# Kernel optimization log

Hardware: AMD Instinct MI355X
Metric: run time of the kernel (lower is better)

The kernel has to match this reference:

```python
import jax, jax.numpy as jnp
import numpy as np

N_NODES = 100000
N_EDGES = 1600000
IN_FEAT = 256
HIDDEN = 64
N_CLASSES = 16


def gcn_conv(x, edge_index, W, b):
    """PyG GCNConv: add self-loops, symmetric normalization, linear+aggregate."""
    n = x.shape[0]
    src, dst = edge_index[0], edge_index[1]
    loops = jnp.arange(n, dtype=src.dtype)
    src = jnp.concatenate([src, loops])
    dst = jnp.concatenate([dst, loops])
    # in-degree on graph with self-loops
    deg = jax.ops.segment_sum(jnp.ones(src.shape[0], dtype=x.dtype), dst, num_segments=n)
    dinv = jnp.where(deg > 0, jax.lax.rsqrt(deg), 0.0)
    h = x @ W                                  # [N, out]
    norm = dinv[src] * dinv[dst]               # [E+N]
    msg = h[src] * norm[:, None]                # gather + scale (memory-bound)
    out = jax.ops.segment_sum(msg, dst, num_segments=n)  # scatter-add
    return out + b


def setup_inputs() -> dict:
    key = jax.random.key(0)
    ks = jax.random.split(key, 5)
    x = jax.random.normal(ks[0], (N_NODES, IN_FEAT), dtype=jnp.float32)
    edge_index = jax.random.randint(ks[1], (2, N_EDGES), 0, N_NODES, dtype=jnp.int64)
    W1 = jax.random.normal(ks[2], (IN_FEAT, HIDDEN), dtype=jnp.float32) * (1.0 / np.sqrt(IN_FEAT))
    b1 = jnp.zeros((HIDDEN,), dtype=jnp.float32)
    W2 = jax.random.normal(ks[3], (HIDDEN, N_CLASSES), dtype=jnp.float32) * (1.0 / np.sqrt(HIDDEN))
    b2 = jnp.zeros((N_CLASSES,), dtype=jnp.float32)
    return {"x": x, "edge_index": edge_index, "W1": W1, "b1": b1, "W2": W2, "b2": b2}


def reference(x, edge_index, W1, b1, W2, b2):
    h = gcn_conv(x, edge_index, W1, b1)
    h = jax.nn.relu(h)
    # dropout p=0.5 is identity in eval mode (training=False)
    out = gcn_conv(h, edge_index, W2, b2)
    return out
```

## Files before the change

kernel.cpp:

```cpp
#include <hip/hip_runtime.h>

#define NN 100000
#define NE 1600000
#define FIN 256
#define FH 64
#define FC 16

#define SCAN_CHUNK 1024
#define NB_SCAN ((NN + SCAN_CHUNK - 1) / SCAN_CHUNK)
#define NB_COUNT ((NE / 4 + 255) / 256)
#define NB_GEMM1 ((NN + 127) / 128)
#define NB_FUSED (3 * NB_GEMM1)

typedef int v2i __attribute__((ext_vector_type(2)));
typedef int v4i __attribute__((ext_vector_type(4)));
typedef short s16x8 __attribute__((ext_vector_type(8)));
typedef float f32x4 __attribute__((ext_vector_type(4)));

__device__ __forceinline__ float4 fma4(float4 v, float w, float4 a) {
    a.x = fmaf(v.x, w, a.x); a.y = fmaf(v.y, w, a.y);
    a.z = fmaf(v.z, w, a.z); a.w = fmaf(v.w, w, a.w);
    return a;
}
__device__ __forceinline__ float4 add4(float4 a, float4 v) {
    a.x += v.x; a.y += v.y; a.z += v.z; a.w += v.w;
    return a;
}
__device__ __forceinline__ float4 xor_add4(float4 r, int m) {
    r.x += __shfl_xor(r.x, m, 64); r.y += __shfl_xor(r.y, m, 64);
    r.z += __shfl_xor(r.z, m, 64); r.w += __shfl_xor(r.w, m, 64);
    return r;
}

__device__ __forceinline__ unsigned short bf16rne(float f) {
    unsigned u = __float_as_uint(f);
    u += 0x7FFFu + ((u >> 16) & 1u);
    return (unsigned short)(u >> 16);
}

__device__ __forceinline__ void split8(const float* f, s16x8& hi, s16x8& lo) {
    #pragma unroll
    for (int i = 0; i < 8; i++) {
        unsigned u = __float_as_uint(f[i]);
        unsigned short h = (unsigned short)((u + 0x7FFFu + ((u >> 16) & 1u)) >> 16);
        float l = f[i] - __uint_as_float((unsigned)h << 16);
        unsigned ul = __float_as_uint(l);
        hi[i] = (short)h;
        lo[i] = (short)((ul + 0x7FFFu + ((ul >> 16) & 1u)) >> 16);
    }
}

__global__ __launch_bounds__(256) void prep_k(const int* __restrict__ ei,
                                              int* __restrict__ flag,
                                              const float* __restrict__ W,
                                              unsigned short* __restrict__ Whi,
                                              unsigned short* __restrict__ Wlo) {
    int b = blockIdx.x;
    if (b == 8) {
        if (threadIdx.x == 0) {
            int z = (ei[1] == 0) & (ei[3] == 0) & (ei[5] == 0) & (ei[7] == 0);
            *flag = z;
        }
        return;
    }
    int slot = b * 256 + threadIdx.x;
    int l = slot & 63;
    int c = (slot >> 6) & 3;
    int s = slot >> 8;
    int k0 = s * 32 + (l >> 4) * 8;
    int col = c * 16 + (l & 15);
    #pragma unroll
    for (int i = 0; i < 8; i++) {
        float f = W[(k0 + i) * FH + col];
        unsigned short h = bf16rne(f);
        float lres = f - __uint_as_float((unsigned)h << 16);
        Whi[slot * 8 + i] = h;
        Wlo[slot * 8 + i] = bf16rne(lres);
    }
}

__global__ __launch_bounds__(256, 4) void fused_k(const int* __restrict__ ei,
                                                  const int* __restrict__ flag,
                                                  int* __restrict__ deg,
                                                  v2i* __restrict__ packed,
                                                  const float* __restrict__ x,
                                                  const unsigned short* __restrict__ Whi,
                                                  const unsigned short* __restrict__ Wlo,
                                                  float* __restrict__ h1) {
    const int b = blockIdx.x;
    if ((b % 3) != 2) {
        int cb = (b / 3) * 2 + (b % 3);
        if (cb >= NB_COUNT) return;
        int e = (cb * 256 + threadIdx.x) * 4;
        if (e >= NE) return;
        int f = *flag;
        int s0, s1, s2, s3, d0, d1, d2, d3;
        if (f) {
            v4i a = *(const v4i*)&ei[2 * e];
            v4i b2 = *(const v4i*)&ei[2 * e + 4];
            s0 = a.x; s1 = a.z; s2 = b2.x; s3 = b2.z;
            v4i c = *(const v4i*)&ei[2 * (NE + e)];
            v4i d = *(const v4i*)&ei[2 * (NE + e) + 4];
            d0 = c.x; d1 = c.z; d2 = d.x; d3 = d.z;
        } else {
            v4i a = *(const v4i*)&ei[e];
            s0 = a.x; s1 = a.y; s2 = a.z; s3 = a.w;
            v4i c = *(const v4i*)&ei[NE + e];
            d0 = c.x; d1 = c.y; d2 = c.z; d3 = c.w;
        }
        int r0 = atomicAdd(&deg[d0], 1);
        int r1 = atomicAdd(&deg[d1], 1);
        int r2 = atomicAdd(&deg[d2], 1);
        int r3 = atomicAdd(&deg[d3], 1);
        v4i pa, pb;
        pa.x = s0; pa.y = d0 | (r0 << 17);
        pa.z = s1; pa.w = d1 | (r1 << 17);
        pb.x = s2; pb.y = d2 | (r2 << 17);
        pb.z = s3; pb.w = d3 | (r3 << 17);
        *(v4i*)&packed[e] = pa;
        *(v4i*)&packed[e + 2] = pb;
        return;
    }
    const int t = threadIdx.x;
    const int lane = t & 63;
    const int wid = t >> 6;
    const int mb = (b / 3) * 128 + wid * 32;
    const int lr = lane & 15;
    const int lk = (lane >> 4) * 8;

    int ra0 = mb + lr;
    int ra1 = mb + 16 + lr;
    const float* pa0 = x + (size_t)(ra0 < NN ? ra0 : NN - 1) * FIN + lk;
    const float* pa1 = x + (size_t)(ra1 < NN ? ra1 : NN - 1) * FIN + lk;

    f32x4 acc[2][4] = {};

    for (int s = 0; s < 8; s++) {
        float fa0[8], fa1[8];
        float4 q;
        q = *(const float4*)(pa0 + s * 32);
        fa0[0] = q.x; fa0[1] = q.y; fa0[2] = q.z; fa0[3] = q.w;
        q = *(const float4*)(pa0 + s * 32 + 4);
        fa0[4] = q.x; fa0[5] = q.y; fa0[6] = q.z; fa0[7] = q.w;
        q = *(const float4*)(pa1 + s * 32);
        fa1[0] = q.x; fa1[1] = q.y; fa1[2] = q.z; fa1[3] = q.w;
        q = *(const float4*)(pa1 + s * 32 + 4);
        fa1[4] = q.x; fa1[5] = q.y; fa1[6] = q.z; fa1[7] = q.w;

        s16x8 a0h, a0l, a1h, a1l;
        split8(fa0, a0h, a0l);
        split8(fa1, a1h, a1l);

        #pragma unroll
        for (int c = 0; c < 4; c++) {
            s16x8 wh = *(const s16x8*)&Whi[((s * 4 + c) * 64 + lane) * 8];
            s16x8 wl = *(const s16x8*)&Wlo[((s * 4 + c) * 64 + lane) * 8];
            acc[0][c] = __builtin_amdgcn_mfma_f32_16x16x32_bf16(a0h, wh, acc[0][c], 0, 0, 0);
            acc[0][c] = __builtin_amdgcn_mfma_f32_16x16x32_bf16(a0l, wh, acc[0][c], 0, 0, 0);
            acc[0][c] = __builtin_amdgcn_mfma_f32_16x16x32_bf16(a0h, wl, acc[0][c], 0, 0, 0);
            acc[1][c] = __builtin_amdgcn_mfma_f32_16x16x32_bf16(a1h, wh, acc[1][c], 0, 0, 0);
            acc[1][c] = __builtin_amdgcn_mfma_f32_16x16x32_bf16(a1l, wh, acc[1][c], 0, 0, 0);
            acc[1][c] = __builtin_amdgcn_mfma_f32_16x16x32_bf16(a1h, wl, acc[1][c], 0, 0, 0);
        }
    }
    #pragma unroll
    for (int r = 0; r < 2; r++) {
        int rowb = mb + 16 * r + (lane >> 4) * 4;
        #pragma unroll
        for (int c = 0; c < 4; c++) {
            #pragma unroll
            for (int v = 0; v < 4; v++) {
                int row = rowb + v;
                if (row < NN)
                    h1[(size_t)row * FH + 16 * c + lr] = acc[r][c][v];
            }
        }
    }
}

__global__ __launch_bounds__(256) void scan_sum_k(const int* __restrict__ deg,
                                                  int* __restrict__ partial,
                                                  float* __restrict__ dinv,
                                                  float* __restrict__ h1) {
    __shared__ int red[256];
    __shared__ float sdv[SCAN_CHUNK];
    int b = blockIdx.x, t = threadIdx.x;
    int base = b * SCAN_CHUNK + t * 4;
    int s = 0;
    #pragma unroll
    for (int i = 0; i < 4; i++) {
        int idx = base + i;
        float dv = 0.f;
        if (idx < NN) {
            int d = deg[idx];
            s += d;
            dv = rsqrtf((float)(d + 1));
            dinv[idx] = dv;
        }
        sdv[t * 4 + i] = dv;
    }
    red[t] = s;
    __syncthreads();
    #pragma unroll 4
    for (int it = 0; it < 64; it++) {
        int q = it * 256 + t;
        int rl = q >> 4;
        int row = b * SCAN_CHUNK + rl;
        if (row < NN) {
            float d = sdv[rl];
            float4 v = *(const float4*)&h1[(size_t)row * FH + (q & 15) * 4];
            v.x *= d; v.y *= d; v.z *= d; v.w *= d;
            *(float4*)&h1[(size_t)row * FH + (q & 15) * 4] = v;
        }
    }
    for (int off = 128; off > 0; off >>= 1) {
        if (t < off) red[t] += red[t + off];
        __syncthreads();
    }
    if (t == 0) partial[b] = red[0];
}

__global__ __launch_bounds__(128) void scan_part_k(int* __restrict__ partial) {
    __shared__ int s[128];
    int t = threadIdx.x;
    int v = (t < NB_SCAN) ? partial[t] : 0;
    s[t] = v; __syncthreads();
    for (int off = 1; off < 128; off <<= 1) {
        int u = (t >= off) ? s[t - off] : 0;
        __syncthreads();
        s[t] += u;
        __syncthreads();
    }
    if (t < NB_SCAN) partial[t] = s[t] - v;
}

__global__ __launch_bounds__(256) void scan_out_k(const int* __restrict__ deg,
                                                  const int* __restrict__ partial,
                                                  int* __restrict__ row_start) {
    __shared__ int s[256];
    int b = blockIdx.x, t = threadIdx.x;
    int base = b * SCAN_CHUNK + t * 4;
    int v[4]; int sum = 0;
    #pragma unroll
    for (int i = 0; i < 4; i++) {
        int idx = base + i;
        v[i] = (idx < NN) ? deg[idx] : 0;
        sum += v[i];
    }
    s[t] = sum; __syncthreads();
    for (int off = 1; off < 256; off <<= 1) {
        int u = (t >= off) ? s[t - off] : 0;
        __syncthreads();
        s[t] += u;
        __syncthreads();
    }
    int run = partial[b] + s[t] - sum;
    #pragma unroll
    for (int i = 0; i < 4; i++) {
        int idx = base + i;
        if (idx < NN) {
            row_start[idx] = run;
            run += v[i];
            if (idx == NN - 1) row_start[NN] = run;
        }
    }
}

__global__ __launch_bounds__(256) void fill_k(const int* __restrict__ packed,
                                              const int* __restrict__ row_start,
                                              int* __restrict__ csr) {
    int e = (blockIdx.x * 256 + threadIdx.x) * 2;
    if (e >= NE) return;
    v4i p = __builtin_nontemporal_load((const v4i*)&packed[2 * e]);
    int d0 = p.y & 0x1FFFF;
    int r0 = ((unsigned)p.y) >> 17;
    int d1 = p.w & 0x1FFFF;
    int r1 = ((unsigned)p.w) >> 17;
    csr[row_start[d0] + r0] = p.x;
    csr[row_start[d1] + r1] = p.z;
}

__global__ __launch_bounds__(256) void agg1g_k(const int* __restrict__ csr,
                                               const int* __restrict__ row_start,
                                               const float* __restrict__ h1,
                                               const float* __restrict__ dinv,
                                               const float* __restrict__ b1,
                                               const float* __restrict__ W2,
                                               float* __restrict__ h2) {
    __shared__ float sW2[FH * FC];
    __shared__ float sp[4][FH];
    const int t = threadIdx.x;
    #pragma unroll
    for (int i = 0; i < 4; i++) sW2[t + 256 * i] = W2[t + 256 * i];
    __syncthreads();

    int wid = t >> 6;
    int n = blockIdx.x * 4 + wid;
    int lane = t & 63;
    if (n >= NN) return;
    int sg = lane >> 4;
    int fl = lane & 15;
    int s0 = row_start[n], s1 = row_start[n + 1];
    float4 A = make_float4(0.f, 0.f, 0.f, 0.f);
    float4 B = make_float4(0.f, 0.f, 0.f, 0.f);
    float4 C = make_float4(0.f, 0.f, 0.f, 0.f);
    float4 D = make_float4(0.f, 0.f, 0.f, 0.f);
    for (int j0 = s0; j0 < s1; j0 += 64) {
        int idx = j0 + lane;
        int sl = (idx < s1) ? csr[idx] : 0;
        int cnt = s1 - j0; if (cnt > 64) cnt = 64;
        int j = 0;
        for (; j + 16 <= cnt; j += 16) {
            int eA = __shfl(sl, j + sg, 64);
            int eB = __shfl(sl, j + 4 + sg, 64);
            int eC = __shfl(sl, j + 8 + sg, 64);
            int eD = __shfl(sl, j + 12 + sg, 64);
            float4 vA = *(const float4*)&h1[eA * FH + fl * 4];
            float4 vB = *(const float4*)&h1[eB * FH + fl * 4];
            float4 vC = *(const float4*)&h1[eC * FH + fl * 4];
            float4 vD = *(const float4*)&h1[eD * FH + fl * 4];
            A = add4(A, vA); B = add4(B, vB);
            C = add4(C, vC); D = add4(D, vD);
        }
        if (j + 8 <= cnt) {
            int eA = __shfl(sl, j + sg, 64);
            int eB = __shfl(sl, j + 4 + sg, 64);
            float4 vA = *(const float4*)&h1[eA * FH + fl * 4];
            float4 vB = *(const float4*)&h1[eB * FH + fl * 4];
            A = add4(A, vA); B = add4(B, vB);
            j += 8;
        }
        if (j + 4 <= cnt) {
            int eA = __shfl(sl, j + sg, 64);
            float4 vA = *(const float4*)&h1[eA * FH + fl * 4];
            A = add4(A, vA);
            j += 4;
        }
        int rem = cnt - j;
        if (rem > 0) {
            int jj = j + (sg < rem ? sg : 0);
            int eA = __shfl(sl, jj, 64);
            float wA = (sg < rem) ? 1.f : 0.f;
            float4 vA = *(const float4*)&h1[eA * FH + fl * 4];
            A = fma4(vA, wA, A);
        }
    }
    float4 r = add4(add4(A, B), add4(C, D));
    r = xor_add4(r, 16);
    r = xor_add4(r, 32);
    float dn = dinv[n];
    if (sg == 0) {
        float4 self = *(const float4*)&h1[n * FH + fl * 4];
        float4 bq = *(const float4*)&b1[fl * 4];
        float4 p;
        p.x = fmaxf(fmaf(r.x + self.x, dn, bq.x), 0.f);
        p.y = fmaxf(fmaf(r.y + self.y, dn, bq.y), 0.f);
        p.z = fmaxf(fmaf(r.z + self.z, dn, bq.z), 0.f);
        p.w = fmaxf(fmaf(r.w + self.w, dn, bq.w), 0.f);
        *(float4*)&sp[wid][fl * 4] = p;
    }
    __builtin_amdgcn_s_waitcnt(0);
    if (lane < FC) {
        float o = 0.f;
        #pragma unroll 8
        for (int k = 0; k < FH; k++)
            o = fmaf(sp[wid][k], sW2[k * FC + lane], o);
        h2[n * FC + lane] = o * dn;
    }
}

__global__ __launch_bounds__(256) void agg2_k(const int* __restrict__ csr,
                                              const int* __restrict__ row_start,
                                              const float* __restrict__ h2,
                                              const float* __restrict__ dinv,
                                              const float* __restrict__ b2,
                                              float* __restrict__ out) {
    const int t = threadIdx.x;
    int n = blockIdx.x * 16 + (t >> 4);
    int l16 = t & 15;
    int base = t & 48;
    int q = (t >> 2) & 3;
    int c = t & 3;
    if (n >= NN) return;
    int s0 = row_start[n], s1 = row_start[n + 1];
    float4 A = make_float4(0.f, 0.f, 0.f, 0.f);
    float4 B = make_float4(0.f, 0.f, 0.f, 0.f);
    float4 C = make_float4(0.f, 0.f, 0.f, 0.f);
    float4 D = make_float4(0.f, 0.f, 0.f, 0.f);
    for (int j0 = s0; j0 < s1; j0 += 16) {
        int idx = j0 + l16;
        int sl = (idx < s1) ? csr[idx] : 0;
        int cnt = s1 - j0; if (cnt > 16) cnt = 16;
        int j = 0;
        if (j + 16 <= cnt) {
            int eA = __shfl(sl, base + j + q, 64);
            int eB = __shfl(sl, base + j + 4 + q, 64);
            int eC = __shfl(sl, base + j + 8 + q, 64);
            int eD = __shfl(sl, base + j + 12 + q, 64);
            float4 vA = *(const float4*)&h2[eA * FC + c * 4];
            float4 vB = *(const float4*)&h2[eB * FC + c * 4];
            float4 vC = *(const float4*)&h2[eC * FC + c * 4];
            float4 vD = *(const float4*)&h2[eD * FC + c * 4];
            A = add4(A, vA); B = add4(B, vB);
            C = add4(C, vC); D = add4(D, vD);
            j += 16;
        }
        if (j + 8 <= cnt) {
            int eA = __shfl(sl, base + j + q, 64);
            int eB = __shfl(sl, base + j + 4 + q, 64);
            float4 vA = *(const float4*)&h2[eA * FC + c * 4];
            float4 vB = *(const float4*)&h2[eB * FC + c * 4];
            A = add4(A, vA); B = add4(B, vB);
            j += 8;
        }
        if (j + 4 <= cnt) {
            int eA = __shfl(sl, base + j + q, 64);
            float4 vA = *(const float4*)&h2[eA * FC + c * 4];
            A = add4(A, vA);
            j += 4;
        }
        int rem = cnt - j;
        if (rem > 0) {
            int jj = base + j + (q < rem ? q : 0);
            int eA = __shfl(sl, jj, 64);
            float wA = (q < rem) ? 1.f : 0.f;
            float4 vA = *(const float4*)&h2[eA * FC + c * 4];
            A = fma4(vA, wA, A);
        }
    }
    float4 r = add4(add4(A, B), add4(C, D));
    r = xor_add4(r, 4);
    r = xor_add4(r, 8);
    if (q == 0) {
        float dn = dinv[n];
        float4 self = *(const float4*)&h2[n * FC + c * 4];
        float4 bq = *(const float4*)&b2[c * 4];
        float4 p;
        p.x = fmaf(r.x + self.x, dn, bq.x);
        p.y = fmaf(r.y + self.y, dn, bq.y);
        p.z = fmaf(r.z + self.z, dn, bq.z);
        p.w = fmaf(r.w + self.w, dn, bq.w);
        *(float4*)&out[n * FC + c * 4] = p;
    }
}

extern "C" void kernel_launch(void* const* d_in, const int* in_sizes, int n_in,
                              void* d_out, int out_size, void* d_ws, size_t ws_size,
                              hipStream_t stream) {
    const float* x  = (const float*)d_in[0];
    const int*   ei = (const int*)d_in[1];
    const float* W1 = (const float*)d_in[2];
    const float* b1 = (const float*)d_in[3];
    const float* W2 = (const float*)d_in[4];
    const float* b2 = (const float*)d_in[5];
    float* out = (float*)d_out;

    char* ws = (char*)d_ws;
    int*   deg       = (int*)(ws + 0);
    int*   row_start = (int*)(ws + 512 * 1024);
    float* dinv      = (float*)(ws + 1024 * 1024);
    int*   flag      = (int*)(ws + 1536 * 1024);
    int*   partial   = (int*)(ws + 1540 * 1024);
    unsigned short* Whi = (unsigned short*)(ws + 1544 * 1024);
    unsigned short* Wlo = (unsigned short*)(ws + 1584 * 1024);
    int*   csr       = (int*)(ws + 2ull * 1024 * 1024);
    float* h1        = (float*)(ws + 9ull * 1024 * 1024);
    v2i*   packed    = (v2i*)(ws + 35ull * 1024 * 1024);
    float* h2        = (float*)(ws + 35ull * 1024 * 1024);

    prep_k<<<9, 256, 0, stream>>>(ei, flag, W1, Whi, Wlo);
    (void)hipMemsetAsync(deg, 0, NN * sizeof(int), stream);
    fused_k<<<NB_FUSED, 256, 0, stream>>>(ei, flag, deg, packed, x, Whi, Wlo, h1);
    scan_sum_k<<<NB_SCAN, 256, 0, stream>>>(deg, partial, dinv, h1);
    scan_part_k<<<1, 128, 0, stream>>>(partial);
    scan_out_k<<<NB_SCAN, 256, 0, stream>>>(deg, partial, row_start);
    fill_k<<<(NE / 2 + 255) / 256, 256, 0, stream>>>((const int*)packed, row_start, csr);

    agg1g_k<<<(NN + 3) / 4, 256, 0, stream>>>(csr, row_start, h1, dinv, b1, W2, h2);
    agg2_k<<<(NN + 15) / 16, 256, 0, stream>>>(csr, row_start, h2, dinv, b2, out);
}
```

Measured before the change: 368.9 us.

## Replicate degree counters eight ways to reduce atomic contention in CSR build

The in-degree histogram is split into eight replicas chosen per wavefront, which spreads the atomic increments across more addresses. Edge packing now also encodes the replica index, and the scan emits one row-start entry per node per replica so that CSR fill can place each edge within its node's segment. The cost is a larger memset (8x the degree array), eight reads per node in the scan kernels, and a row_start array eight times as large, which the aggregation kernels index with stride 8.

After: 364.4 us. No clear change (-1.2%).

```diff
diff --git a/kernel.cpp b/kernel.cpp
--- a/kernel.cpp
+++ b/kernel.cpp
@@ -5,9 +5,9 @@
 #define FIN 256
 #define FH 64
 #define FC 16
-
-#define SCAN_CHUNK 1024
-#define NB_SCAN ((NN + SCAN_CHUNK - 1) / SCAN_CHUNK)
+#define K_REP 8
+
+#define NB_SCAN2 ((NN + 255) / 256)
 #define NB_COUNT ((NE / 4 + 255) / 256)
 #define NB_GEMM1 ((NN + 127) / 128)
 #define NB_FUSED (3 * NB_GEMM1)
@@ -81,7 +81,7 @@
 
 __global__ __launch_bounds__(256, 4) void fused_k(const int* __restrict__ ei,
                                                   const int* __restrict__ flag,
-                                                  int* __restrict__ deg,
+                                                  int* __restrict__ deg2,
                                                   v2i* __restrict__ packed,
                                                   const float* __restrict__ x,
                                                   const unsigned short* __restrict__ Whi,
@@ -93,6 +93,7 @@
         if (cb >= NB_COUNT) return;
         int e = (cb * 256 + threadIdx.x) * 4;
         if (e >= NE) return;
+        int kk = ((cb << 2) | (threadIdx.x >> 6)) & 7;
         int f = *flag;
         int s0, s1, s2, s3, d0, d1, d2, d3;
         if (f) {
@@ -108,15 +109,17 @@
             v4i c = *(const v4i*)&ei[NE + e];
             d0 = c.x; d1 = c.y; d2 = c.z; d3 = c.w;
         }
-        int r0 = atomicAdd(&deg[d0], 1);
-        int r1 = atomicAdd(&deg[d1], 1);
-        int r2 = atomicAdd(&deg[d2], 1);
-        int r3 = atomicAdd(&deg[d3], 1);
+        int* dg = deg2 + kk * NN;
+        int r0 = atomicAdd(&dg[d0], 1);
+        int r1 = atomicAdd(&dg[d1], 1);
+        int r2 = atomicAdd(&dg[d2], 1);
+        int r3 = atomicAdd(&dg[d3], 1);
+        int kb = kk << 17;
         v4i pa, pb;
-        pa.x = s0; pa.y = d0 | (r0 << 17);
-        pa.z = s1; pa.w = d1 | (r1 << 17);
-        pb.x = s2; pb.y = d2 | (r2 << 17);
-        pb.z = s3; pb.w = d3 | (r3 << 17);
+        pa.x = s0; pa.y = d0 | kb | (r0 << 20);
+        pa.z = s1; pa.w = d1 | kb | (r1 << 20);
+        pb.x = s2; pb.y = d2 | kb | (r2 << 20);
+        pb.z = s3; pb.w = d3 | kb | (r3 << 20);
         *(v4i*)&packed[e] = pa;
         *(v4i*)&packed[e + 2] = pb;
         return;
@@ -178,34 +181,30 @@
     }
 }
 
-__global__ __launch_bounds__(256) void scan_sum_k(const int* __restrict__ deg,
+__global__ __launch_bounds__(256) void scan_sum_k(const int* __restrict__ deg2,
                                                   int* __restrict__ partial,
                                                   float* __restrict__ dinv,
                                                   float* __restrict__ h1) {
     __shared__ int red[256];
-    __shared__ float sdv[SCAN_CHUNK];
+    __shared__ float sdv[256];
     int b = blockIdx.x, t = threadIdx.x;
-    int base = b * SCAN_CHUNK + t * 4;
-    int s = 0;
-    #pragma unroll
-    for (int i = 0; i < 4; i++) {
-        int idx = base + i;
-        float dv = 0.f;
-        if (idx < NN) {
-            int d = deg[idx];
-            s += d;
-            dv = rsqrtf((float)(d + 1));
-            dinv[idx] = dv;
-        }
-        sdv[t * 4 + i] = dv;
-    }
-    red[t] = s;
+    int n = b * 256 + t;
+    int sum = 0;
+    float dv = 0.f;
+    if (n < NN) {
+        #pragma unroll
+        for (int k = 0; k < K_REP; k++) sum += deg2[k * NN + n];
+        dv = rsqrtf((float)(sum + 1));
+        dinv[n] = dv;
+    }
+    sdv[t] = dv;
+    red[t] = sum;
     __syncthreads();
     #pragma unroll 4
-    for (int it = 0; it < 64; it++) {
+    for (int it = 0; it < 16; it++) {
         int q = it * 256 + t;
         int rl = q >> 4;
-        int row = b * SCAN_CHUNK + rl;
+        int row = b * 256 + rl;
         if (row < NN) {
             float d = sdv[rl];
             float4 v = *(const float4*)&h1[(size_t)row * FH + (q & 15) * 4];
@@ -220,32 +219,31 @@
     if (t == 0) partial[b] = red[0];
 }
 
-__global__ __launch_bounds__(128) void scan_part_k(int* __restrict__ partial) {
-    __shared__ int s[128];
+__global__ __launch_bounds__(512) void scan_part_k(int* __restrict__ partial) {
+    __shared__ int s[512];
     int t = threadIdx.x;
-    int v = (t < NB_SCAN) ? partial[t] : 0;
+    int v = (t < NB_SCAN2) ? partial[t] : 0;
     s[t] = v; __syncthreads();
-    for (int off = 1; off < 128; off <<= 1) {
+    for (int off = 1; off < 512; off <<= 1) {
         int u = (t >= off) ? s[t - off] : 0;
         __syncthreads();
         s[t] += u;
         __syncthreads();
     }
-    if (t < NB_SCAN) partial[t] = s[t] - v;
-}
-
-__global__ __launch_bounds__(256) void scan_out_k(const int* __restrict__ deg,
+    if (t < NB_SCAN2) partial[t] = s[t] - v;
+}
+
+__global__ __launch_bounds__(256) void scan_out_k(const int* __restrict__ deg2,
                                                   const int* __restrict__ partial,
                                                   int* __restrict__ row_start) {
     __shared__ int s[256];
     int b = blockIdx.x, t = threadIdx.x;
-    int base = b * SCAN_CHUNK + t * 4;
-    int v[4]; int sum = 0;
+    int n = b * 256 + t;
+    int v[K_REP]; int sum = 0;
     #pragma unroll
-    for (int i = 0; i < 4; i++) {
-        int idx = base + i;
-        v[i] = (idx < NN) ? deg[idx] : 0;
-        sum += v[i];
+    for (int k = 0; k < K_REP; k++) {
+        v[k] = (n < NN) ? deg2[k * NN + n] : 0;
+        sum += v[k];
     }
     s[t] = sum; __syncthreads();
     for (int off = 1; off < 256; off <<= 1) {
@@ -255,14 +253,13 @@
         __syncthreads();
     }
     int run = partial[b] + s[t] - sum;
-    #pragma unroll
-    for (int i = 0; i < 4; i++) {
-        int idx = base + i;
-        if (idx < NN) {
-            row_start[idx] = run;
-            run += v[i];
-            if (idx == NN - 1) row_start[NN] = run;
-        }
+    if (n < NN) {
+        #pragma unroll
+        for (int k = 0; k < K_REP; k++) {
+            row_start[n * K_REP + k] = run;
+            run += v[k];
+        }
+        if (n == NN - 1) row_start[NN * K_REP] = run;
     }
 }
 
@@ -273,11 +270,13 @@
     if (e >= NE) return;
     v4i p = __builtin_nontemporal_load((const v4i*)&packed[2 * e]);
     int d0 = p.y & 0x1FFFF;
-    int r0 = ((unsigned)p.y) >> 17;
+    int k0 = (p.y >> 17) & 7;
+    int r0 = ((unsigned)p.y) >> 20;
     int d1 = p.w & 0x1FFFF;
-    int r1 = ((unsigned)p.w) >> 17;
-    csr[row_start[d0] + r0] = p.x;
-    csr[row_start[d1] + r1] = p.z;
+    int k1 = (p.w >> 17) & 7;
+    int r1 = ((unsigned)p.w) >> 20;
+    csr[row_start[d0 * K_REP + k0] + r0] = p.x;
+    csr[row_start[d1 * K_REP + k1] + r1] = p.z;
 }
 
 __global__ __launch_bounds__(256) void agg1g_k(const int* __restrict__ csr,
@@ -300,7 +299,7 @@
     if (n >= NN) return;
     int sg = lane >> 4;
     int fl = lane & 15;
-    int s0 = row_start[n], s1 = row_start[n + 1];
+    int s0 = row_start[n * K_REP], s1 = row_start[n * K_REP + K_REP];
     float4 A = make_float4(0.f, 0.f, 0.f, 0.f);
     float4 B = make_float4(0.f, 0.f, 0.f, 0.f);
     float4 C = make_float4(0.f, 0.f, 0.f, 0.f);
@@ -382,7 +381,7 @@
     int q = (t >> 2) & 3;
     int c = t & 3;
     if (n >= NN) return;
-    int s0 = row_start[n], s1 = row_start[n + 1];
+    int s0 = row_start[n * K_REP], s1 = row_start[n * K_REP + K_REP];
     float4 A = make_float4(0.f, 0.f, 0.f, 0.f);
     float4 B = make_float4(0.f, 0.f, 0.f, 0.f);
     float4 C = make_float4(0.f, 0.f, 0.f, 0.f);
@@ -456,24 +455,24 @@
     float* out = (float*)d_out;
 
     char* ws = (char*)d_ws;
-    int*   deg       = (int*)(ws + 0);
-    int*   row_start = (int*)(ws + 512 * 1024);
-    float* dinv      = (float*)(ws + 1024 * 1024);
-    int*   flag      = (int*)(ws + 1536 * 1024);
-    int*   partial   = (int*)(ws + 1540 * 1024);
-    unsigned short* Whi = (unsigned short*)(ws + 1544 * 1024);
-    unsigned short* Wlo = (unsigned short*)(ws + 1584 * 1024);
-    int*   csr       = (int*)(ws + 2ull * 1024 * 1024);
-    float* h1        = (float*)(ws + 9ull * 1024 * 1024);
-    v2i*   packed    = (v2i*)(ws + 35ull * 1024 * 1024);
-    float* h2        = (float*)(ws + 35ull * 1024 * 1024);
+    int*   row_start = (int*)(ws + 0);
+    float* dinv      = (float*)(ws + 3400ull * 1024);
+    int*   flag      = (int*)(ws + 3800ull * 1024);
+    int*   partial   = (int*)(ws + 3804ull * 1024);
+    unsigned short* Whi = (unsigned short*)(ws + 3840ull * 1024);
+    unsigned short* Wlo = (unsigned short*)(ws + 3904ull * 1024);
+    int*   deg2      = (int*)(ws + 4096ull * 1024);
+    int*   csr       = (int*)(ws + 4096ull * 1024);
+    float* h1        = (float*)(ws + 10400ull * 1024);
+    v2i*   packed    = (v2i*)(ws + 35400ull * 1024);
+    float* h2        = (float*)(ws + 35400ull * 1024);
 
     prep_k<<<9, 256, 0, stream>>>(ei, flag, W1, Whi, Wlo);
-    (void)hipMemsetAsync(deg, 0, NN * sizeof(int), stream);
-    fused_k<<<NB_FUSED, 256, 0, stream>>>(ei, flag, deg, packed, x, Whi, Wlo, h1);
-    scan_sum_k<<<NB_SCAN, 256, 0, stream>>>(deg, partial, dinv, h1);
-    scan_part_k<<<1, 128, 0, stream>>>(partial);
-    scan_out_k<<<NB_SCAN, 256, 0, stream>>>(deg, partial, row_start);
+    (void)hipMemsetAsync(deg2, 0, (size_t)K_REP * NN * sizeof(int), stream);
+    fused_k<<<NB_FUSED, 256, 0, stream>>>(ei, flag, deg2, packed, x, Whi, Wlo, h1);
+    scan_sum_k<<<NB_SCAN2, 256, 0, stream>>>(deg2, partial, dinv, h1);
+    scan_part_k<<<1, 512, 0, stream>>>(partial);
+    scan_out_k<<<NB_SCAN2, 256, 0, stream>>>(deg2, partial, row_start);
     fill_k<<<(NE / 2 + 255) / 256, 256, 0, stream>>>((const int*)packed, row_start, csr);
 
     agg1g_k<<<(NN + 3) / 4, 256, 0, stream>>>(csr, row_start, h1, dinv, b1, W2, h2);
```
